# Optimization experiments

Measured on AMD Instinct MI355X. Metric: run time of the kernel, lower is better.

## Reference

```python
import jax, jax.numpy as jnp
import numpy as np

B, L, D, F = 8, 1024, 256, 11
TEMP = D ** 0.5
LN_EPS = 1e-6


def setup_inputs() -> dict:
    key = jax.random.key(0)
    ks = jax.random.split(key, 14)
    mk = lambda k, s: jax.random.normal(k, s, dtype=jnp.float32)
    return {
        "q": mk(ks[0], (B, L, D)),
        "k": mk(ks[1], (B, L, D)),
        "v": mk(ks[2], (B, L, D)),
        "x": jax.random.uniform(ks[3], (B, L, F), dtype=jnp.float32),
        "inputs_lengths": jax.random.randint(ks[4], (B,), 512, L + 1),
        "w_qs": mk(ks[5], (D, D)) * 0.05,
        "w_ks": mk(ks[6], (D, D)) * 0.05,
        "w_vs": mk(ks[7], (D, D)) * 0.05,
        "w_qs2": mk(ks[8], (D, D)) * 0.05,
        "w_ks2": mk(ks[9], (D, D)) * 0.05,
        "w_fc": mk(ks[10], (D, D)) * 0.05,
        "feature_importance": mk(ks[11], (F,)) * 0.1,
        "ln_gamma": jnp.ones((D,), jnp.float32),
        "ln_beta": jnp.zeros((D,), jnp.float32),
    }


def reference(q, k, v, x, w_qs, w_ks, w_vs, w_qs2, w_ks2, w_fc,
              feature_importance, ln_gamma, ln_beta, inputs_lengths):
    lin = lambda a, w: jnp.einsum('bli,oi->blo', a, w)  # torch Linear: y = x W^T
    qp = lin(q, w_qs)
    kp = lin(k, w_ks)
    vp = lin(v, w_vs)
    q2 = lin(q, w_qs2)
    k2 = lin(k, w_ks2)

    # key-position validity mask [B, L]
    key_mask = jnp.arange(L)[None, :] < inputs_lengths[:, None]

    # FeatureSim: pairwise L1 feature distances weighted by feature_importance
    fd = jnp.abs(x[:, :, None, :] - x[:, None, :, :])           # [B,L,L,F]
    fa = jnp.einsum('bijf,f->bij', fd, feature_importance)      # [B,L,L]
    fa = jnp.where(key_mask[:, None, :], fa, -jnp.inf)          # pad_masking
    fa = jax.nn.softmax(fa, axis=-1)
    fa = jnp.nan_to_num(fa)                                     # nan -> 0 for fully-masked rows

    # dual-score attention with tanh activation (no row normalization)
    attn = jnp.einsum('bid,bjd->bij', qp / TEMP, kp)
    q2f = jnp.einsum('bij,bjd->bid', fa, q2)
    k2f = jnp.einsum('bij,bjd->bid', fa, k2)
    attn = attn + jnp.einsum('bid,bjd->bij', q2f / TEMP, k2f)
    zm = key_mask[:, None, :]
    attn = jnp.where(zm, attn, 0.0)                             # pad_zero_masking
    attn = jnp.tanh(attn)
    attn = jnp.where(zm, attn, 0.0)                             # pad_zero_masking (tanh(0)=0, kept for fidelity)

    out = jnp.einsum('bij,bjd->bid', attn, vp)
    out = lin(out, w_fc) + q                                    # dropout is identity at eval
    mu = jnp.mean(out, axis=-1, keepdims=True)
    var = jnp.var(out, axis=-1, keepdims=True)
    out = (out - mu) / jnp.sqrt(var + LN_EPS) * ln_gamma + ln_beta
    return (out, attn)
```

## Files before the change

kernel.cpp:

```cpp
#include <hip/hip_runtime.h>
#include <hip/hip_bf16.h>
#include <math.h>

typedef __hip_bfloat16 bf16;
typedef __bf16 bf16x8 __attribute__((ext_vector_type(8)));
typedef float  f32x4  __attribute__((ext_vector_type(4)));

#define NB 8
#define SL 1024
#define DD 256
#define NF 11
#define RPB 8

#define AS_G __attribute__((address_space(1)))
#define AS_L __attribute__((address_space(3)))

__device__ __forceinline__ bf16x8 ldfrag(const bf16* p) {
  return *reinterpret_cast<const bf16x8*>(p);
}
__device__ __forceinline__ bf16x8 ldfrag(const float* p) {
  const float4 a = *reinterpret_cast<const float4*>(p);
  const float4 b = *reinterpret_cast<const float4*>(p + 4);
  bf16x8 r;
  r[0] = (__bf16)a.x; r[1] = (__bf16)a.y; r[2] = (__bf16)a.z; r[3] = (__bf16)a.w;
  r[4] = (__bf16)b.x; r[5] = (__bf16)b.y; r[6] = (__bf16)b.z; r[7] = (__bf16)b.w;
  return r;
}
__device__ __forceinline__ unsigned short us(float f) {
  bf16 h = __float2bfloat16(f);
  return *reinterpret_cast<unsigned short*>(&h);
}
__device__ __forceinline__ float tanh_fast(float x) {
  return 1.f - 2.f / (__expf(2.f * x) + 1.f);
}

template<int R>
__device__ __forceinline__ void stage_t(const float* __restrict__ g, int ld,
                                        bf16* __restrict__ s, int tid) {
#pragma unroll
  for (int it = 0; it < R / 32; ++it) {
    const int cid = it * 256 + tid;
    const int row = cid >> 3, c16 = cid & 7;
    bf16x8 v = ldfrag(g + (size_t)row * ld + c16 * 8);
    *reinterpret_cast<bf16x8*>(s + row * 64 + ((c16 ^ (row & 7)) << 3)) = v;
  }
}
template<int R>
__device__ __forceinline__ void stage_t(const bf16* __restrict__ g, int ld,
                                        bf16* __restrict__ s, int tid) {
  const int wbase = tid & ~63;
#pragma unroll
  for (int it = 0; it < R / 32; ++it) {
    const int cid = it * 256 + tid;
    const int row = cid >> 3, sc = cid & 7;
    const int c16 = sc ^ (row & 7);
    const bf16* src = g + (size_t)row * ld + c16 * 8;
    bf16* dst = s + (size_t)(it * 256 + wbase) * 8;
    __builtin_amdgcn_global_load_lds((const AS_G void*)src, (AS_L void*)dst, 16, 0, 0);
  }
}

__device__ __forceinline__ void compute_128x128(const bf16* __restrict__ sA,
                                                const bf16* __restrict__ sB,
                                                int lane, int wave, f32x4 acc[4][4]) {
  const int n15 = lane & 15, quad = lane >> 4;
  const int wr = (wave >> 1) << 6, wc = (wave & 1) << 6;
#pragma unroll
  for (int kc = 0; kc < 2; ++kc) {
    const int c16 = kc * 4 + quad;
    bf16x8 aF[4], bF[4];
#pragma unroll
    for (int t = 0; t < 4; ++t) {
      const int ra = wr + t * 16 + n15;
      aF[t] = *reinterpret_cast<const bf16x8*>(sA + ra * 64 + ((c16 ^ (ra & 7)) << 3));
      const int rb = wc + t * 16 + n15;
      bF[t] = *reinterpret_cast<const bf16x8*>(sB + rb * 64 + ((c16 ^ (rb & 7)) << 3));
    }
#pragma unroll
    for (int ti = 0; ti < 4; ++ti)
#pragma unroll
      for (int tj = 0; tj < 4; ++tj)
        acc[ti][tj] = __builtin_amdgcn_mfma_f32_16x16x32_bf16(aF[ti], bF[tj], acc[ti][tj], 0, 0, 0);
  }
}

__device__ __forceinline__ void compute_32x256(const bf16* __restrict__ sA,
                                               const bf16* __restrict__ sB,
                                               int lane, int wave, f32x4 acc[2][4]) {
  const int n15 = lane & 15, quad = lane >> 4;
  const int wc = wave << 6;
#pragma unroll
  for (int kc = 0; kc < 2; ++kc) {
    const int c16 = kc * 4 + quad;
    bf16x8 aF[2], bF[4];
#pragma unroll
    for (int t = 0; t < 2; ++t) {
      const int ra = t * 16 + n15;
      aF[t] = *reinterpret_cast<const bf16x8*>(sA + ra * 64 + ((c16 ^ (ra & 7)) << 3));
    }
#pragma unroll
    for (int t = 0; t < 4; ++t) {
      const int rb = wc + t * 16 + n15;
      bF[t] = *reinterpret_cast<const bf16x8*>(sB + rb * 64 + ((c16 ^ (rb & 7)) << 3));
    }
#pragma unroll
    for (int ti = 0; ti < 2; ++ti)
#pragma unroll
      for (int tj = 0; tj < 4; ++tj)
        acc[ti][tj] = __builtin_amdgcn_mfma_f32_16x16x32_bf16(aF[ti], bF[tj], acc[ti][tj], 0, 0, 0);
  }
}

template<typename TA, typename TB>
__device__ __forceinline__ void gemm_128x128(const TA* __restrict__ A, int lda,
                                             const TB* __restrict__ B, int ldb, int K,
                                             bf16* s, int tid, f32x4 acc[4][4]) {
  const int lane = tid & 63, wave = tid >> 6;
  stage_t<128>(A, lda, s, tid);
  stage_t<128>(B, ldb, s + 8192, tid);
  int cur = 0;
  __syncthreads();
  for (int k0 = 0; k0 < K; k0 += 64) {
    bf16* sc0 = s + cur * 16384;
    if (k0 + 64 < K) {
      bf16* sn = s + (cur ^ 1) * 16384;
      stage_t<128>(A + k0 + 64, lda, sn, tid);
      stage_t<128>(B + k0 + 64, ldb, sn + 8192, tid);
    }
    compute_128x128(sc0, sc0 + 8192, lane, wave, acc);
    __syncthreads();
    cur ^= 1;
  }
}

__device__ __forceinline__ float wred_sum(float v) {
#pragma unroll
  for (int o = 32; o > 0; o >>= 1) v += __shfl_xor(v, o, 64);
  return v;
}

__global__ __launch_bounds__(256) void k_fp(
    const float* __restrict__ q, const float* __restrict__ k, const float* __restrict__ v,
    const float* __restrict__ x, const float* __restrict__ fi_g,
    const int* __restrict__ lens,
    const float* __restrict__ wqs, const float* __restrict__ wks,
    const float* __restrict__ wvs, const float* __restrict__ wqs2,
    const float* __restrict__ wks2,
    bf16* __restrict__ qq, bf16* __restrict__ kk,
    bf16* __restrict__ vpt, bf16* __restrict__ q2t, bf16* __restrict__ k2t,
    bf16* __restrict__ fa)
{
  __shared__ __align__(16) char pool[65536];
  const int tid = threadIdx.x, lane = tid & 63, wave = tid >> 6;
  const int bid = blockIdx.x;
  if (bid < 640) {
    bf16* smem = (bf16*)pool;
    const int z = bid >> 7, sub = bid & 127;
    const int rowBase = (sub & 63) * 128;
    const int colBase = (sub >> 6) * 128;
    const float* A = (z == 2) ? v : ((z == 1 || z == 4) ? k : q);
    const float* W = (z == 0) ? wqs : (z == 1) ? wks : (z == 2) ? wvs : (z == 3) ? wqs2 : wks2;
    f32x4 acc[4][4] = {};
    gemm_128x128(A + (size_t)rowBase * DD, DD, W + (size_t)colBase * DD, DD, DD, smem, tid, acc);
    const int n15 = lane & 15, quad = lane >> 4;
    const int wr = (wave >> 1) << 6, wc = (wave & 1) << 6;
    if (z <= 1) {
      bf16* O = (z == 0) ? qq : kk;
#pragma unroll
      for (int ti = 0; ti < 4; ++ti)
#pragma unroll
        for (int tj = 0; tj < 4; ++tj)
#pragma unroll
          for (int r = 0; r < 4; ++r) {
            int row = rowBase + wr + ti * 16 + quad * 4 + r;
            int col = colBase + wc + tj * 16 + n15;
            O[(size_t)row * 512 + col] = __float2bfloat16(acc[ti][tj][r]);
          }
    } else {
      bf16* O = (z == 2) ? vpt : (z == 3) ? q2t : k2t;
      const int bb = rowBase >> 10, rowInB = rowBase & 1023;
#pragma unroll
      for (int ti = 0; ti < 4; ++ti)
#pragma unroll
        for (int tj = 0; tj < 4; ++tj) {
          int l0  = rowInB + wr + ti * 16 + quad * 4;
          int col = colBase + wc + tj * 16 + n15;
          ushort4 pk = make_ushort4(us(acc[ti][tj][0]), us(acc[ti][tj][1]),
                                    us(acc[ti][tj][2]), us(acc[ti][tj][3]));
          *reinterpret_cast<ushort4*>(&O[((size_t)bb * DD + col) * SL + l0]) = pk;
        }
    }
    return;
  }
  float* sx = (float*)pool;
  float* sredS = (float*)(pool + 45056);
  const int fid = bid - 640;
  const int b  = fid >> 7;
  const int i0 = (fid & 127) * RPB;
  {
    const float4* src = reinterpret_cast<const float4*>(x + (size_t)b * SL * NF);
    float4* dst = reinterpret_cast<float4*>(sx);
#pragma unroll
    for (int it = 0; it < 11; ++it) dst[it * 256 + tid] = src[it * 256 + tid];
  }
  float fiv[NF];
#pragma unroll
  for (int f = 0; f < NF; ++f) fiv[f] = fi_g[f];
  const int len = lens[b];
  __syncthreads();
  float xi[RPB][NF];
#pragma unroll
  for (int i = 0; i < RPB; ++i)
#pragma unroll
    for (int f = 0; f < NF; ++f) xi[i][f] = sx[(i0 + i) * NF + f];
  float e[RPB][4];
  float ps[RPB];
#pragma unroll
  for (int i = 0; i < RPB; ++i) ps[i] = 0.f;
#pragma unroll
  for (int t = 0; t < 4; ++t) {
    const int j = tid + t * 256;
    const bool valid = (t < 2) || (j < len);
    float xj[NF];
#pragma unroll
    for (int f = 0; f < NF; ++f) xj[f] = sx[j * NF + f];
#pragma unroll
    for (int i = 0; i < RPB; ++i) {
      float a = 0.f;
#pragma unroll
      for (int f = 0; f < NF; ++f) a += fabsf(xi[i][f] - xj[f]) * fiv[f];
      float ev = valid ? __expf(a) : 0.f;
      e[i][t] = ev;
      ps[i] += ev;
    }
  }
#pragma unroll
  for (int i = 0; i < RPB; ++i) {
    float wsv = wred_sum(ps[i]);
    if ((tid & 63) == 0) sredS[wave * RPB + i] = wsv;
  }
  __syncthreads();
  bf16* out = fa + (size_t)b * SL * SL + (size_t)i0 * SL;
#pragma unroll
  for (int i = 0; i < RPB; ++i) {
    const float inv = 1.f / (sredS[0 * RPB + i] + sredS[1 * RPB + i] +
                             sredS[2 * RPB + i] + sredS[3 * RPB + i]);
#pragma unroll
    for (int t = 0; t < 4; ++t)
      out[(size_t)i * SL + tid + t * 256] = __float2bfloat16(e[i][t] * inv);
  }
}

__global__ __launch_bounds__(256) void k_famul(const bf16* __restrict__ fa,
                                               const bf16* __restrict__ q2t,
                                               const bf16* __restrict__ k2t,
                                               const int* __restrict__ lens,
                                               bf16* __restrict__ qq,
                                               bf16* __restrict__ kk)
{
  __shared__ bf16 smem[32768];
  const int tid = threadIdx.x, lane = tid & 63, wave = tid >> 6;
  const int flat = blockIdx.x + 8 * blockIdx.y + 16 * blockIdx.z;
  const int lid  = (flat & 7) * 32 + (flat >> 3);
  const int bx = lid & 7, by = (lid >> 3) & 1, bz = lid >> 4;
  const int b = bz >> 1, which = bz & 1;
  const int iBase = bx * 128, dBase = by * 128;
  const int Keff = (lens[b] + 63) & ~63;
  const bf16* A  = fa + (size_t)b * SL * SL + (size_t)iBase * SL;
  const bf16* Bm = (which ? k2t : q2t) + (size_t)b * DD * SL + (size_t)dBase * SL;
  f32x4 acc[4][4] = {};
  gemm_128x128(A, SL, Bm, SL, Keff, smem, tid, acc);
  bf16* O = (which ? kk : qq) + (size_t)b * SL * 512 + 256;
  const int n15 = lane & 15, quad = lane >> 4;
  const int wr = (wave >> 1) << 6, wc = (wave & 1) << 6;
#pragma unroll
  for (int ti = 0; ti < 4; ++ti)
#pragma unroll
    for (int tj = 0; tj < 4; ++tj)
#pragma unroll
      for (int r = 0; r < 4; ++r)
        O[(size_t)(iBase + wr + ti * 16 + quad * 4 + r) * 512 +
          dBase + wc + tj * 16 + n15] = __float2bfloat16(acc[ti][tj][r]);
}

__global__ __launch_bounds__(256) void k_attn(const bf16* __restrict__ qq,
                                              const bf16* __restrict__ kk,
                                              const int* __restrict__ lens,
                                              float* __restrict__ attn_f32,
                                              bf16* __restrict__ attn_b16)
{
  __shared__ bf16 smem[32768];
  const int tid = threadIdx.x, lane = tid & 63, wave = tid >> 6;
  const int flat = blockIdx.x + 8 * blockIdx.y + 64 * blockIdx.z;
  const int lid  = (flat & 7) * 64 + (flat >> 3);
  const int bx = lid & 7, by = (lid >> 3) & 7, bz = lid >> 6;
  const int b = bz;
  const int iBase = bx * 128, jBase = by * 128;
  const int len = lens[b];
  if (jBase >= len) {
    const int r = tid >> 1, ch = (tid & 1) * 64;
    float* pf = attn_f32 + (size_t)b * SL * SL + (size_t)(iBase + r) * SL + jBase + ch;
    bf16*  pb = attn_b16 + (size_t)b * SL * SL + (size_t)(iBase + r) * SL + jBase + ch;
    const float4 z4 = make_float4(0.f, 0.f, 0.f, 0.f);
    const uint4  zb = make_uint4(0u, 0u, 0u, 0u);
#pragma unroll
    for (int i = 0; i < 16; ++i) *reinterpret_cast<float4*>(pf + i * 4) = z4;
#pragma unroll
    for (int i = 0; i < 8; ++i)  *reinterpret_cast<uint4*>(pb + i * 8) = zb;
    return;
  }
  f32x4 acc[4][4] = {};
  gemm_128x128(qq + ((size_t)b * SL + iBase) * 512, 512,
               kk + ((size_t)b * SL + jBase) * 512, 512, 512, smem, tid, acc);
  const int n15 = lane & 15, quad = lane >> 4;
  const int wr = (wave >> 1) << 6, wc = (wave & 1) << 6;
#pragma unroll
  for (int ti = 0; ti < 4; ++ti)
#pragma unroll
    for (int tj = 0; tj < 4; ++tj)
#pragma unroll
      for (int r = 0; r < 4; ++r) {
        int i = iBase + wr + ti * 16 + quad * 4 + r;
        int j = jBase + wc + tj * 16 + n15;
        float vv = (j < len) ? tanh_fast(acc[ti][tj][r] * (1.f / 16.f)) : 0.f;
        size_t idx = (size_t)b * SL * SL + (size_t)i * SL + j;
        attn_f32[idx] = vv;
        attn_b16[idx] = __float2bfloat16(vv);
      }
}

__global__ __launch_bounds__(256) void k_avln(const bf16* __restrict__ attn,
                                              const bf16* __restrict__ vpt,
                                              const float* __restrict__ qres,
                                              const float* __restrict__ wfc,
                                              const int* __restrict__ lens,
                                              const float* __restrict__ gam,
                                              const float* __restrict__ bet,
                                              float* __restrict__ outp)
{
  __shared__ bf16 smem[36864];
  const int tid = threadIdx.x, lane = tid & 63, wave = tid >> 6;
  const int flat = blockIdx.x;
  const int lid  = (flat & 7) * 32 + (flat >> 3);
  const int b = lid >> 5, bx = lid & 31;
  const int iBase = bx * 32;
  const int Keff = (lens[b] + 63) & ~63;
  const bf16* A  = attn + (size_t)b * SL * SL + (size_t)iBase * SL;
  const bf16* Bm = vpt + (size_t)b * DD * SL;
  f32x4 acc[2][4] = {};
  {
    stage_t<32>(A, SL, smem, tid);
    stage_t<256>(Bm, SL, smem + 2048, tid);
    int cur = 0;
    __syncthreads();
    for (int k0 = 0; k0 < Keff; k0 += 64) {
      bf16* sc = smem + cur * 18432;
      if (k0 + 64 < Keff) {
        bf16* sn = smem + (cur ^ 1) * 18432;
        stage_t<32>(A + k0 + 64, SL, sn, tid);
        stage_t<256>(Bm + k0 + 64, SL, sn + 2048, tid);
      }
      compute_32x256(sc, sc + 2048, lane, wave, acc);
      __syncthreads();
      cur ^= 1;
    }
  }
  const int n15 = lane & 15, quad = lane >> 4;
  bf16* sY  = smem;
  bf16* sB2 = smem + 8192;
#pragma unroll
  for (int ti = 0; ti < 2; ++ti)
#pragma unroll
    for (int tj = 0; tj < 4; ++tj)
#pragma unroll
      for (int r = 0; r < 4; ++r) {
        const int row = ti * 16 + quad * 4 + r;
        const int cc  = tj * 16 + n15;
        sY[wave * 2048 + row * 64 + (((cc >> 3) ^ (row & 7)) << 3) + (cc & 7)] =
            __float2bfloat16(acc[ti][tj][r]);
      }
  stage_t<256>(wfc, DD, sB2, tid);
  __syncthreads();
  f32x4 acc2[2][4] = {};
#pragma unroll 1
  for (int kb = 0; kb < 4; ++kb) {
    compute_32x256(sY + kb * 2048, sB2, lane, wave, acc2);
    __syncthreads();
    if (kb < 3) {
      stage_t<256>(wfc + (kb + 1) * 64, DD, sB2, tid);
      __syncthreads();
    }
  }
  const int wcol = wave << 6;
  float val[2][4][4];
  float sS_p[2][4], sQ_p[2][4];
#pragma unroll
  for (int ti = 0; ti < 2; ++ti)
#pragma unroll
    for (int r = 0; r < 4; ++r) {
      const size_t grow = (size_t)b * SL + iBase + ti * 16 + quad * 4 + r;
      float s = 0.f, ss = 0.f;
#pragma unroll
      for (int tj = 0; tj < 4; ++tj) {
        const int col = wcol + tj * 16 + n15;
        float vv = acc2[ti][tj][r] + qres[grow * DD + col];
        val[ti][tj][r] = vv;
        s += vv; ss += vv * vv;
      }
      sS_p[ti][r] = s; sQ_p[ti][r] = ss;
    }
#pragma unroll
  for (int o = 8; o > 0; o >>= 1)
#pragma unroll
    for (int ti = 0; ti < 2; ++ti)
#pragma unroll
      for (int r = 0; r < 4; ++r) {
        sS_p[ti][r] += __shfl_xor(sS_p[ti][r], o, 64);
        sQ_p[ti][r] += __shfl_xor(sQ_p[ti][r], o, 64);
      }
  float* sS = (float*)smem;
  float* sQ = sS + 4 * 32;
  if (n15 == 0) {
#pragma unroll
    for (int ti = 0; ti < 2; ++ti)
#pragma unroll
      for (int r = 0; r < 4; ++r) {
        const int rloc = ti * 16 + quad * 4 + r;
        sS[wave * 32 + rloc] = sS_p[ti][r];
        sQ[wave * 32 + rloc] = sQ_p[ti][r];
      }
  }
  __syncthreads();
#pragma unroll
  for (int ti = 0; ti < 2; ++ti)
#pragma unroll
    for (int r = 0; r < 4; ++r) {
      const int rloc = ti * 16 + quad * 4 + r;
      const float s  = sS[rloc] + sS[32 + rloc] + sS[64 + rloc] + sS[96 + rloc];
      const float ss = sQ[rloc] + sQ[32 + rloc] + sQ[64 + rloc] + sQ[96 + rloc];
      const float mean = s * (1.f / DD);
      const float var  = ss * (1.f / DD) - mean * mean;
      const float rstd = rsqrtf(var + 1e-6f);
      const size_t grow = (size_t)b * SL + iBase + rloc;
#pragma unroll
      for (int tj = 0; tj < 4; ++tj) {
        const int col = wcol + tj * 16 + n15;
        const float y = (val[ti][tj][r] - mean) * rstd * gam[col] + bet[col];
        outp[grow * DD + col] = y;
      }
    }
}

extern "C" void kernel_launch(void* const* d_in, const int* in_sizes, int n_in,
                              void* d_out, int out_size, void* d_ws, size_t ws_size,
                              hipStream_t stream)
{
  const float* q    = (const float*)d_in[0];
  const float* k    = (const float*)d_in[1];
  const float* v    = (const float*)d_in[2];
  const float* x    = (const float*)d_in[3];
  const int*  lens  = (const int*)d_in[4];
  const float* wqs  = (const float*)d_in[5];
  const float* wks  = (const float*)d_in[6];
  const float* wvs  = (const float*)d_in[7];
  const float* wqs2 = (const float*)d_in[8];
  const float* wks2 = (const float*)d_in[9];
  const float* wfc  = (const float*)d_in[10];
  const float* fi   = (const float*)d_in[11];
  const float* gam  = (const float*)d_in[12];
  const float* bet  = (const float*)d_in[13];

  char* w = (char*)d_ws;
  const size_t MB = 1u << 20;
  bf16* qq    = (bf16*)(w + 0 * MB);
  bf16* kk    = (bf16*)(w + 8 * MB);
  bf16* vpt   = (bf16*)(w + 16 * MB);
  bf16* q2t   = (bf16*)(w + 20 * MB);
  bf16* k2t   = (bf16*)(w + 24 * MB);
  bf16* fa    = (bf16*)(w + 28 * MB);
  bf16* attn_b16 = fa;

  float* outp  = (float*)d_out;
  float* attnp = outp + (size_t)NB * SL * DD;

  dim3 blk(256);
  hipLaunchKernelGGL(k_fp,    dim3(640 + NB * 128), blk, 0, stream,
                     q, k, v, x, fi, lens, wqs, wks, wvs, wqs2, wks2,
                     qq, kk, vpt, q2t, k2t, fa);
  hipLaunchKernelGGL(k_famul, dim3(8, 2, 16),  blk, 0, stream, fa, q2t, k2t, lens, qq, kk);
  hipLaunchKernelGGL(k_attn,  dim3(8, 8, 8),   blk, 0, stream,
                     qq, kk, lens, attnp, attn_b16);
  hipLaunchKernelGGL(k_avln,  dim3(256),       blk, 0, stream,
                     attn_b16, vpt, q, wfc, lens, gam, bet, outp);
}
```

Baseline: 182.0 us.

## Drop bf16 attention copy and remap famul blocks to XCD-local groups

The attention kernel no longer writes a second bf16 copy of the attention matrix. The AV/LayerNorm kernel now reads the fp32 attention output directly, relying on the float overload of ldfrag to convert on load, which removes a large write stream. The famul kernel uses a 1D grid whose block index is remapped so the four blocks sharing one fa row-tile land on the same XCD, aiming for better L2 reuse. The trade-off is that the AV kernel reads twice the bytes for attention, and its staging code must handle float inputs.

```diff
diff --git a/kernel.cpp b/kernel.cpp
--- a/kernel.cpp
+++ b/kernel.cpp
@@ -260,10 +260,12 @@
 {
   __shared__ bf16 smem[32768];
   const int tid = threadIdx.x, lane = tid & 63, wave = tid >> 6;
-  const int flat = blockIdx.x + 8 * blockIdx.y + 16 * blockIdx.z;
-  const int lid  = (flat & 7) * 32 + (flat >> 3);
-  const int bx = lid & 7, by = (lid >> 3) & 1, bz = lid >> 4;
-  const int b = bz >> 1, which = bz & 1;
+  const int flat = blockIdx.x;
+  const int xcd = flat & 7, slot = flat >> 3;
+  const int p = slot & 3, ghi = slot >> 2;
+  const int g = ghi * 8 + xcd;
+  const int b = g >> 3, bx = g & 7;
+  const int by = p >> 1, which = p & 1;
   const int iBase = bx * 128, dBase = by * 128;
   const int Keff = (lens[b] + 63) & ~63;
   const bf16* A  = fa + (size_t)b * SL * SL + (size_t)iBase * SL;
@@ -286,8 +288,7 @@
 __global__ __launch_bounds__(256) void k_attn(const bf16* __restrict__ qq,
                                               const bf16* __restrict__ kk,
                                               const int* __restrict__ lens,
-                                              float* __restrict__ attn_f32,
-                                              bf16* __restrict__ attn_b16)
+                                              float* __restrict__ attn_f32)
 {
   __shared__ bf16 smem[32768];
   const int tid = threadIdx.x, lane = tid & 63, wave = tid >> 6;
@@ -300,13 +301,9 @@
   if (jBase >= len) {
     const int r = tid >> 1, ch = (tid & 1) * 64;
     float* pf = attn_f32 + (size_t)b * SL * SL + (size_t)(iBase + r) * SL + jBase + ch;
-    bf16*  pb = attn_b16 + (size_t)b * SL * SL + (size_t)(iBase + r) * SL + jBase + ch;
     const float4 z4 = make_float4(0.f, 0.f, 0.f, 0.f);
-    const uint4  zb = make_uint4(0u, 0u, 0u, 0u);
 #pragma unroll
     for (int i = 0; i < 16; ++i) *reinterpret_cast<float4*>(pf + i * 4) = z4;
-#pragma unroll
-    for (int i = 0; i < 8; ++i)  *reinterpret_cast<uint4*>(pb + i * 8) = zb;
     return;
   }
   f32x4 acc[4][4] = {};
@@ -323,13 +320,11 @@
         int i = iBase + wr + ti * 16 + quad * 4 + r;
         int j = jBase + wc + tj * 16 + n15;
         float vv = (j < len) ? tanh_fast(acc[ti][tj][r] * (1.f / 16.f)) : 0.f;
-        size_t idx = (size_t)b * SL * SL + (size_t)i * SL + j;
-        attn_f32[idx] = vv;
-        attn_b16[idx] = __float2bfloat16(vv);
-      }
-}
-
-__global__ __launch_bounds__(256) void k_avln(const bf16* __restrict__ attn,
+        attn_f32[(size_t)b * SL * SL + (size_t)i * SL + j] = vv;
+      }
+}
+
+__global__ __launch_bounds__(256) void k_avln(const float* __restrict__ attn,
                                               const bf16* __restrict__ vpt,
                                               const float* __restrict__ qres,
                                               const float* __restrict__ wfc,
@@ -345,7 +340,7 @@
   const int b = lid >> 5, bx = lid & 31;
   const int iBase = bx * 32;
   const int Keff = (lens[b] + 63) & ~63;
-  const bf16* A  = attn + (size_t)b * SL * SL + (size_t)iBase * SL;
+  const float* A = attn + (size_t)b * SL * SL + (size_t)iBase * SL;
   const bf16* Bm = vpt + (size_t)b * DD * SL;
   f32x4 acc[2][4] = {};
   {
@@ -478,7 +473,6 @@
   bf16* q2t   = (bf16*)(w + 20 * MB);
   bf16* k2t   = (bf16*)(w + 24 * MB);
   bf16* fa    = (bf16*)(w + 28 * MB);
-  bf16* attn_b16 = fa;
 
   float* outp  = (float*)d_out;
   float* attnp = outp + (size_t)NB * SL * DD;
@@ -487,9 +481,8 @@
   hipLaunchKernelGGL(k_fp,    dim3(640 + NB * 128), blk, 0, stream,
                      q, k, v, x, fi, lens, wqs, wks, wvs, wqs2, wks2,
                      qq, kk, vpt, q2t, k2t, fa);
-  hipLaunchKernelGGL(k_famul, dim3(8, 2, 16),  blk, 0, stream, fa, q2t, k2t, lens, qq, kk);
-  hipLaunchKernelGGL(k_attn,  dim3(8, 8, 8),   blk, 0, stream,
-                     qq, kk, lens, attnp, attn_b16);
-  hipLaunchKernelGGL(k_avln,  dim3(256),       blk, 0, stream,
-                     attn_b16, vpt, q, wfc, lens, gam, bet, outp);
-}
+  hipLaunchKernelGGL(k_famul, dim3(256),      blk, 0, stream, fa, q2t, k2t, lens, qq, kk);
+  hipLaunchKernelGGL(k_attn,  dim3(8, 8, 8),  blk, 0, stream, qq, kk, lens, attnp);
+  hipLaunchKernelGGL(k_avln,  dim3(256),      blk, 0, stream,
+                     attnp, vpt, q, wfc, lens, gam, bet, outp);
+}
```

After: 183.7 us. No clear change (+1.0%).
